# Kernel tuning notes

Measured on AMD Instinct MI355X. Metric: run time of the kernel, lower is better.

The kernel has to match this reference:

```python
import jax, jax.numpy as jnp
import numpy as np

N_FILTERS = 64
COV_EPS = 1e-4
ALPHA = 0.1  # cov_shrinkage_alpha

_tri_r, _tri_c = np.triu_indices(N_FILTERS)
_TRI_R = jnp.asarray(_tri_r)
_TRI_C = jnp.asarray(_tri_c)
_TRI_SCALE = jnp.where(_TRI_R != _TRI_C, np.sqrt(2.0), 1.0).astype(jnp.float32)


def setup_inputs() -> dict:
    key = jax.random.key(0)
    k1, k2 = jax.random.split(key)
    x = jax.random.normal(k1, (256, 128, 1, 4096), dtype=jnp.float32)
    # 1x1 conv weight [out_ch, in_ch] (kernel spatial dims are 1x1)
    proj_w = jax.random.normal(k2, (64, 128), dtype=jnp.float32) * 0.05
    return {"x": x, "proj_w": proj_w}


def reference(x, proj_w):
    # 1x1 conv channel projection: [B, Cin, 1, T] -> [B, F, T]
    x = jnp.einsum('bcht,fc->bfht', x, proj_w)[:, :, 0, :].astype(jnp.float32)
    # center over time
    x = x - x.mean(axis=-1, keepdims=True)
    denom = float(max(x.shape[-1] - 1, 1))
    cov = jnp.einsum('bft,bgt->bfg', x, x) / denom  # [B, F, F]
    n = cov.shape[-1]
    eye = jnp.eye(n, dtype=cov.dtype)
    # shrinkage toward scaled identity
    mu = jnp.trace(cov, axis1=-2, axis2=-1) / n  # [B]
    cov = (1.0 - ALPHA) * cov + ALPHA * mu[:, None, None] * eye
    # symmetrize + jitter
    cov = 0.5 * (cov + jnp.swapaxes(cov, -1, -2)) + COV_EPS * eye
    # log-Euclidean map via batched eigh
    eigvals, eigvecs = jnp.linalg.eigh(cov)
    eigvals = jnp.clip(eigvals, COV_EPS)
    log_cov = jnp.einsum('bij,bj,bkj->bik', eigvecs, jnp.log(eigvals), eigvecs)
    log_cov = 0.5 * (log_cov + jnp.swapaxes(log_cov, -1, -2))
    # upper-triangular vectorization with sqrt(2) off-diagonal scaling
    vec = log_cov[:, _TRI_R, _TRI_C] * _TRI_SCALE  # [B, F*(F+1)/2]
    return vec
```

## Files before the change

### kernel.cpp

```cpp
#include <hip/hip_runtime.h>

typedef __attribute__((ext_vector_type(8))) short s8_t;
typedef __attribute__((ext_vector_type(4))) float f4_t;

#define NBATCH 256
#define NCH    128
#define NT     4096
#define NF     64
#define TT     128
#define CHUNKS 4
#define CT     (NT / CHUNKS)
#define NIT    (CT / TT)
#define LDSK   (TT + 8)
#define CHEB_D 20

static __device__ __forceinline__ unsigned short f32_bf16(float f) {
    unsigned int u = __float_as_uint(f);
    return (unsigned short)((u + 0x7FFFu + ((u >> 16) & 1u)) >> 16);
}
static __device__ __forceinline__ float bf16_f32(unsigned short h) {
    return __uint_as_float(((unsigned int)h) << 16);
}

__global__ __launch_bounds__(512, 4)
void k_gram(const float* __restrict__ x, float* __restrict__ gws, float* __restrict__ sxws) {
    __shared__ __align__(16) unsigned short xl[2][NCH * LDSK];
    __shared__ float red[512];

    const int tid  = threadIdx.x;
    const int lane = tid & 63;
    const int wv   = tid >> 6;
    const int bid  = blockIdx.x;
    const int b    = bid >> 2;
    const int chnk = bid & 3;
    const int lrow16 = tid >> 5;
    const int lchunk = tid & 31;

    const float* xb = x + (size_t)b * ((size_t)NCH * NT) + chnk * CT;

    const int arow0 = (wv & 3) * 32;
    const int bcol0 = (wv >> 2) * 64;
    const int lrow  = lane & 15;
    const int koff  = (lane >> 4) * 8;

    f4_t acc[2][4];
    #pragma unroll
    for (int i = 0; i < 2; ++i)
        #pragma unroll
        for (int j = 0; j < 4; ++j)
            acc[i][j] = (f4_t){0.f, 0.f, 0.f, 0.f};

    float sxp = 0.f;
    float4 ld[8];

    #pragma unroll
    for (int j = 0; j < 8; ++j) {
        const int r = j * 16 + lrow16;
        ld[j] = *(const float4*)(xb + (size_t)r * NT + lchunk * 4);
    }
    #pragma unroll
    for (int j = 0; j < 8; ++j) {
        const int r = j * 16 + lrow16;
        ushort4 h;
        h.x = f32_bf16(ld[j].x); h.y = f32_bf16(ld[j].y);
        h.z = f32_bf16(ld[j].z); h.w = f32_bf16(ld[j].w);
        *(ushort4*)&xl[0][r * LDSK + lchunk * 4] = h;
    }
    __syncthreads();

    for (int it = 0; it < NIT; ++it) {
        const int cur = it & 1;
        if (it + 1 < NIT) {
            const int t0 = (it + 1) * TT;
            #pragma unroll
            for (int j = 0; j < 8; ++j) {
                const int r = j * 16 + lrow16;
                ld[j] = *(const float4*)(xb + (size_t)r * NT + t0 + lchunk * 4);
            }
        }
        const unsigned short* bufc = xl[cur];
        #pragma unroll
        for (int ks = 0; ks < TT / 32; ++ks) {
            const int k0 = ks * 32 + koff;
            const s8_t af0 = *(const s8_t*)&bufc[(arow0 + lrow) * LDSK + k0];
            const s8_t af1 = *(const s8_t*)&bufc[(arow0 + 16 + lrow) * LDSK + k0];
            #pragma unroll
            for (int cb = 0; cb < 4; ++cb) {
                const s8_t bf = *(const s8_t*)&bufc[(bcol0 + cb * 16 + lrow) * LDSK + k0];
                acc[0][cb] = __builtin_amdgcn_mfma_f32_16x16x32_bf16(af0, bf, acc[0][cb], 0, 0, 0);
                acc[1][cb] = __builtin_amdgcn_mfma_f32_16x16x32_bf16(af1, bf, acc[1][cb], 0, 0, 0);
            }
        }
        {
            const unsigned short* rp = &bufc[(tid >> 2) * LDSK + (tid & 3) * 32];
            float s = 0.f;
            #pragma unroll
            for (int q = 0; q < 4; ++q) {
                s8_t v = *(const s8_t*)&rp[q * 8];
                #pragma unroll
                for (int e = 0; e < 8; ++e)
                    s += bf16_f32((unsigned short)v[e]);
            }
            sxp += s;
        }
        if (it + 1 < NIT) {
            #pragma unroll
            for (int j = 0; j < 8; ++j) {
                const int r = j * 16 + lrow16;
                ushort4 h;
                h.x = f32_bf16(ld[j].x); h.y = f32_bf16(ld[j].y);
                h.z = f32_bf16(ld[j].z); h.w = f32_bf16(ld[j].w);
                *(ushort4*)&xl[cur ^ 1][r * LDSK + lchunk * 4] = h;
            }
        }
        __syncthreads();
    }

    float* gb = gws + ((size_t)bid << 14);
    const int lrow4 = (lane >> 4) * 4;
    const int lcol  = lane & 15;
    #pragma unroll
    for (int i = 0; i < 2; ++i) {
        const int rbase = arow0 + i * 16 + lrow4;
        #pragma unroll
        for (int cb = 0; cb < 4; ++cb) {
            const int col = bcol0 + cb * 16 + lcol;
            #pragma unroll
            for (int reg = 0; reg < 4; ++reg)
                gb[(size_t)(rbase + reg) * NCH + col] = acc[i][cb][reg];
        }
    }
    red[tid] = sxp;
    __syncthreads();
    if (tid < NCH)
        sxws[bid * NCH + tid] = red[tid * 4] + red[tid * 4 + 1] + red[tid * 4 + 2] + red[tid * 4 + 3];
}

__global__ __launch_bounds__(512, 2)
void k_logm(const float* __restrict__ gws, const float* __restrict__ sxws,
            const float* __restrict__ wmat, float* __restrict__ out) {
    __shared__ __align__(16) float lds[33032];
    float* sG   = lds;
    float* sC0  = lds;
    float* sU   = lds + 4096;
    float* sB0  = lds + 8192;
    float* sB1  = lds + 12288;
    float* sWt  = lds + 16384;
    float* sM1t = lds + 24576;
    float* ssx  = lds + 32768;
    float* sp   = lds + 32896;
    float* sred = lds + 32960;
    float* sscal= lds + 33024;

    const int tid = threadIdx.x;
    const int b   = blockIdx.x;

    for (int i = tid; i < NF * NCH; i += 512) sM1t[i] = wmat[i];
    if (tid < NCH) {
        const float* sxb = sxws + (size_t)b * 4 * NCH;
        ssx[tid] = sxb[tid] + sxb[NCH + tid] + sxb[2 * NCH + tid] + sxb[3 * NCH + tid];
    }
    {
        const float4* g0 = (const float4*)(gws + ((size_t)(b * 4 + 0) << 14));
        const float4* g1 = (const float4*)(gws + ((size_t)(b * 4 + 1) << 14));
        const float4* g2 = (const float4*)(gws + ((size_t)(b * 4 + 2) << 14));
        const float4* g3 = (const float4*)(gws + ((size_t)(b * 4 + 3) << 14));
        float4* dst = (float4*)sG;
        for (int i = tid; i < 4096; i += 512) {
            const float4 a = g0[i], c = g1[i], d = g2[i], e = g3[i];
            float4 r;
            r.x = a.x + c.x + d.x + e.x;
            r.y = a.y + c.y + d.y + e.y;
            r.z = a.z + c.z + d.z + e.z;
            r.w = a.w + c.w + d.w + e.w;
            dst[i] = r;
        }
    }
    __syncthreads();
    for (int i = tid; i < NF * NCH; i += 512) {
        const int f = i >> 7, k = i & 127;
        sWt[k * 64 + f] = sM1t[i];
    }
    __syncthreads();

    {
        const int f0 = (tid >> 5) * 4, c0 = (tid & 31) * 4;
        float a[4][4];
        #pragma unroll
        for (int i = 0; i < 4; ++i)
            #pragma unroll
            for (int j = 0; j < 4; ++j) a[i][j] = 0.f;
        for (int k = 0; k < NCH; ++k) {
            const float4 w4 = *(const float4*)&sWt[k * 64 + f0];
            const float4 g4 = *(const float4*)&sG[k * NCH + c0];
            const float wa[4] = {w4.x, w4.y, w4.z, w4.w};
            const float ga[4] = {g4.x, g4.y, g4.z, g4.w};
            #pragma unroll
            for (int i = 0; i < 4; ++i)
                #pragma unroll
                for (int j = 0; j < 4; ++j)
                    a[i][j] = fmaf(wa[i], ga[j], a[i][j]);
        }
        #pragma unroll
        for (int j = 0; j < 4; ++j) {
            float4 v; v.x = a[0][j]; v.y = a[1][j]; v.z = a[2][j]; v.w = a[3][j];
            *(float4*)&sM1t[(c0 + j) * 64 + f0] = v;
        }
    }
    if (tid < NF) {
        float s = 0.f;
        for (int k = 0; k < NCH; ++k) s = fmaf(sWt[k * 64 + tid], ssx[k], s);
        sp[tid] = s;
    }
    __syncthreads();

    {
        const int f0 = (tid >> 5) * 4, g2 = (tid & 31) * 2;
        float a[4][2];
        #pragma unroll
        for (int i = 0; i < 4; ++i) { a[i][0] = 0.f; a[i][1] = 0.f; }
        for (int k = 0; k < NCH; ++k) {
            const float4 m4 = *(const float4*)&sM1t[k * 64 + f0];
            const float2 w2 = *(const float2*)&sWt[k * 64 + g2];
            const float ma[4] = {m4.x, m4.y, m4.z, m4.w};
            #pragma unroll
            for (int i = 0; i < 4; ++i) {
                a[i][0] = fmaf(ma[i], w2.x, a[i][0]);
                a[i][1] = fmaf(ma[i], w2.y, a[i][1]);
            }
        }
        const float i4096 = 1.f / 4096.f, i4095 = 1.f / 4095.f;
        #pragma unroll
        for (int i = 0; i < 4; ++i)
            #pragma unroll
            for (int j = 0; j < 2; ++j)
                sC0[(f0 + i) * 64 + (g2 + j)] =
                    (a[i][j] - sp[f0 + i] * sp[g2 + j] * i4096) * i4095;
    }
    __syncthreads();

    if (tid == 0) {
        float s = 0.f;
        for (int i = 0; i < 64; ++i) s += sC0[i * 65];
        sscal[0] = s * (1.f / 64.f);
    }
    __syncthreads();

    const float mu = sscal[0];
    const float dshift = 0.1f * mu + 1e-4f;
    for (int i = tid; i < 4096; i += 512) {
        const int r = i >> 6, c = i & 63;
        float v = 0.45f * (sC0[r * 64 + c] + sC0[c * 64 + r]);
        if (r == c) v += dshift;
        sU[i] = v;
    }
    __syncthreads();

    if (tid < 64) {
        float s = 0.f;
        for (int j = 0; j < 64; ++j) s += fabsf(sU[j * 64 + tid]);
        sred[tid] = s;
    }
    __syncthreads();
    if (tid == 0) {
        float hi = 0.f;
        for (int i = 0; i < 64; ++i) hi = fmaxf(hi, sred[i]);
        const float lo = dshift;
        hi = fmaxf(hi, lo * 1.02f);
        float wsc = (hi - lo) / (hi + lo);
        wsc = fminf(fmaxf(wsc, 1e-6f), 0.999999f);
        const float zz = fmaxf((1.f - sqrtf(fmaxf(1.f - wsc * wsc, 1e-12f))) / wsc, 1e-12f);
        const float mc = 0.5f * (hi + lo);
        sscal[1] = mc;
        sscal[2] = wsc;
        sscal[3] = zz;
        sscal[4] = logf(mc) - log1pf(zz * zz);
    }
    __syncthreads();

    {
        const float mc = sscal[1], wsc = sscal[2];
        const float inv_mw = 1.f / (mc * wsc);
        const float inv_w  = 1.f / wsc;
        for (int i = tid; i < 4096; i += 512) {
            const int r = i >> 6, c = i & 63;
            float v = sU[i] * inv_mw;
            if (r == c) v -= inv_w;
            sU[i] = v;
        }
    }
    __syncthreads();

    const int f0 = (tid >> 5) * 4, g2 = (tid & 31) * 2;
    const float zc  = sscal[3];
    const float l2z = log2f(zc);
    float rP[4][2], rP2[4][2];
    {
        const float cd = 2.f * ((CHEB_D & 1) ? 1.f : -1.f) *
                         exp2f((float)CHEB_D * l2z) / (float)CHEB_D;
        #pragma unroll
        for (int i = 0; i < 4; ++i)
            #pragma unroll
            for (int j = 0; j < 2; ++j) {
                rP[i][j]  = (f0 + i == g2 + j) ? cd : 0.f;
                rP2[i][j] = 0.f;
            }
        #pragma unroll
        for (int i = 0; i < 4; ++i) {
            float2 v; v.x = rP[i][0]; v.y = rP[i][1];
            *(float2*)&sB0[(f0 + i) * 64 + g2] = v;
        }
    }
    __syncthreads();

    float* bcur = sB0;
    float* bnxt = sB1;
    for (int k = CHEB_D - 1; k >= 1; --k) {
        const float ck = 2.f * ((k & 1) ? 1.f : -1.f) * exp2f((float)k * l2z) / (float)k;
        float a[4][2];
        #pragma unroll
        for (int i = 0; i < 4; ++i) { a[i][0] = 0.f; a[i][1] = 0.f; }
        #pragma unroll 4
        for (int kk = 0; kk < 64; ++kk) {
            const float4 u4 = *(const float4*)&sU[kk * 64 + f0];
            const float2 b2 = *(const float2*)&bcur[kk * 64 + g2];
            const float ua[4] = {u4.x, u4.y, u4.z, u4.w};
            #pragma unroll
            for (int i = 0; i < 4; ++i) {
                a[i][0] = fmaf(ua[i], b2.x, a[i][0]);
                a[i][1] = fmaf(ua[i], b2.y, a[i][1]);
            }
        }
        #pragma unroll
        for (int i = 0; i < 4; ++i)
            #pragma unroll
            for (int j = 0; j < 2; ++j) {
                const float v = 2.f * a[i][j] - rP2[i][j] + ((f0 + i == g2 + j) ? ck : 0.f);
                rP2[i][j] = rP[i][j];
                rP[i][j]  = v;
            }
        #pragma unroll
        for (int i = 0; i < 4; ++i) {
            float2 v; v.x = rP[i][0]; v.y = rP[i][1];
            *(float2*)&bnxt[(f0 + i) * 64 + g2] = v;
        }
        float* t = bcur; bcur = bnxt; bnxt = t;
        __syncthreads();
    }
    {
        const float c0c = sscal[4];
        float a[4][2];
        #pragma unroll
        for (int i = 0; i < 4; ++i) { a[i][0] = 0.f; a[i][1] = 0.f; }
        #pragma unroll 4
        for (int kk = 0; kk < 64; ++kk) {
            const float4 u4 = *(const float4*)&sU[kk * 64 + f0];
            const float2 b2 = *(const float2*)&bcur[kk * 64 + g2];
            const float ua[4] = {u4.x, u4.y, u4.z, u4.w};
            #pragma unroll
            for (int i = 0; i < 4; ++i) {
                a[i][0] = fmaf(ua[i], b2.x, a[i][0]);
                a[i][1] = fmaf(ua[i], b2.y, a[i][1]);
            }
        }
        #pragma unroll
        for (int i = 0; i < 4; ++i) {
            float2 v;
            v.x = ((f0 + i == g2 + 0) ? c0c : 0.f) + a[i][0] - rP2[i][0];
            v.y = ((f0 + i == g2 + 1) ? c0c : 0.f) + a[i][1] - rP2[i][1];
            *(float2*)&bnxt[(f0 + i) * 64 + g2] = v;
        }
    }
    __syncthreads();
    const float* sF = bnxt;

    float* ob = out + (size_t)b * 2080;
    for (int idx = tid; idx < 2080; idx += 512) {
        const double disc = 16641.0 - 8.0 * (double)idx;
        const int i = (int)((129.0 - sqrt(disc)) * 0.5);
        const int Si = i * 64 - (i * (i - 1)) / 2;
        const int j = i + (idx - Si);
        float v = 0.5f * (sF[i * 64 + j] + sF[j * 64 + i]);
        if (i != j) v *= 1.4142135623730951f;
        ob[idx] = v;
    }
}

extern "C" void kernel_launch(void* const* d_in, const int* in_sizes, int n_in,
                              void* d_out, int out_size, void* d_ws, size_t ws_size,
                              hipStream_t stream) {
    const float* x    = (const float*)d_in[0];
    const float* wmat = (const float*)d_in[1];
    float* outp = (float*)d_out;
    float* gws  = (float*)d_ws;
    float* sxws = gws + (size_t)NBATCH * CHUNKS * NCH * NCH;
    k_gram<<<dim3(NBATCH * CHUNKS), dim3(512), 0, stream>>>(x, gws, sxws);
    k_logm<<<dim3(NBATCH), dim3(512), 0, stream>>>(gws, sxws, wmat, outp);
}
```

Before: 780.1 us.

## Fuse Gram accumulation and log-matrix stage into a single per-batch kernel

Merges the chunked Gram/row-sum kernel and the projection/logm kernel into one kernel with one block per batch. Each block now sweeps the full time axis itself and writes the Gram matrix and channel sums straight into LDS. This removes the global workspace round trip, the cross-chunk reduction and a second launch. In exchange, the memory-bound Gram phase drops from 1024 blocks at four per CU to 256 single-resident blocks, leaving fewer waves to hide global-load latency.

New measurement: 751.8 us. 1.04x faster.

```diff
diff --git a/kernel.cpp b/kernel.cpp
--- a/kernel.cpp
+++ b/kernel.cpp
@@ -8,9 +8,7 @@
 #define NT     4096
 #define NF     64
 #define TT     128
-#define CHUNKS 4
-#define CT     (NT / CHUNKS)
-#define NIT    (CT / TT)
+#define NIT    (NT / TT)
 #define LDSK   (TT + 8)
 #define CHEB_D 20
 
@@ -22,124 +20,11 @@
     return __uint_as_float(((unsigned int)h) << 16);
 }
 
-__global__ __launch_bounds__(512, 4)
-void k_gram(const float* __restrict__ x, float* __restrict__ gws, float* __restrict__ sxws) {
-    __shared__ __align__(16) unsigned short xl[2][NCH * LDSK];
-    __shared__ float red[512];
-
-    const int tid  = threadIdx.x;
-    const int lane = tid & 63;
-    const int wv   = tid >> 6;
-    const int bid  = blockIdx.x;
-    const int b    = bid >> 2;
-    const int chnk = bid & 3;
-    const int lrow16 = tid >> 5;
-    const int lchunk = tid & 31;
-
-    const float* xb = x + (size_t)b * ((size_t)NCH * NT) + chnk * CT;
-
-    const int arow0 = (wv & 3) * 32;
-    const int bcol0 = (wv >> 2) * 64;
-    const int lrow  = lane & 15;
-    const int koff  = (lane >> 4) * 8;
-
-    f4_t acc[2][4];
-    #pragma unroll
-    for (int i = 0; i < 2; ++i)
-        #pragma unroll
-        for (int j = 0; j < 4; ++j)
-            acc[i][j] = (f4_t){0.f, 0.f, 0.f, 0.f};
-
-    float sxp = 0.f;
-    float4 ld[8];
-
-    #pragma unroll
-    for (int j = 0; j < 8; ++j) {
-        const int r = j * 16 + lrow16;
-        ld[j] = *(const float4*)(xb + (size_t)r * NT + lchunk * 4);
-    }
-    #pragma unroll
-    for (int j = 0; j < 8; ++j) {
-        const int r = j * 16 + lrow16;
-        ushort4 h;
-        h.x = f32_bf16(ld[j].x); h.y = f32_bf16(ld[j].y);
-        h.z = f32_bf16(ld[j].z); h.w = f32_bf16(ld[j].w);
-        *(ushort4*)&xl[0][r * LDSK + lchunk * 4] = h;
-    }
-    __syncthreads();
-
-    for (int it = 0; it < NIT; ++it) {
-        const int cur = it & 1;
-        if (it + 1 < NIT) {
-            const int t0 = (it + 1) * TT;
-            #pragma unroll
-            for (int j = 0; j < 8; ++j) {
-                const int r = j * 16 + lrow16;
-                ld[j] = *(const float4*)(xb + (size_t)r * NT + t0 + lchunk * 4);
-            }
-        }
-        const unsigned short* bufc = xl[cur];
-        #pragma unroll
-        for (int ks = 0; ks < TT / 32; ++ks) {
-            const int k0 = ks * 32 + koff;
-            const s8_t af0 = *(const s8_t*)&bufc[(arow0 + lrow) * LDSK + k0];
-            const s8_t af1 = *(const s8_t*)&bufc[(arow0 + 16 + lrow) * LDSK + k0];
-            #pragma unroll
-            for (int cb = 0; cb < 4; ++cb) {
-                const s8_t bf = *(const s8_t*)&bufc[(bcol0 + cb * 16 + lrow) * LDSK + k0];
-                acc[0][cb] = __builtin_amdgcn_mfma_f32_16x16x32_bf16(af0, bf, acc[0][cb], 0, 0, 0);
-                acc[1][cb] = __builtin_amdgcn_mfma_f32_16x16x32_bf16(af1, bf, acc[1][cb], 0, 0, 0);
-            }
-        }
-        {
-            const unsigned short* rp = &bufc[(tid >> 2) * LDSK + (tid & 3) * 32];
-            float s = 0.f;
-            #pragma unroll
-            for (int q = 0; q < 4; ++q) {
-                s8_t v = *(const s8_t*)&rp[q * 8];
-                #pragma unroll
-                for (int e = 0; e < 8; ++e)
-                    s += bf16_f32((unsigned short)v[e]);
-            }
-            sxp += s;
-        }
-        if (it + 1 < NIT) {
-            #pragma unroll
-            for (int j = 0; j < 8; ++j) {
-                const int r = j * 16 + lrow16;
-                ushort4 h;
-                h.x = f32_bf16(ld[j].x); h.y = f32_bf16(ld[j].y);
-                h.z = f32_bf16(ld[j].z); h.w = f32_bf16(ld[j].w);
-                *(ushort4*)&xl[cur ^ 1][r * LDSK + lchunk * 4] = h;
-            }
-        }
-        __syncthreads();
-    }
-
-    float* gb = gws + ((size_t)bid << 14);
-    const int lrow4 = (lane >> 4) * 4;
-    const int lcol  = lane & 15;
-    #pragma unroll
-    for (int i = 0; i < 2; ++i) {
-        const int rbase = arow0 + i * 16 + lrow4;
-        #pragma unroll
-        for (int cb = 0; cb < 4; ++cb) {
-            const int col = bcol0 + cb * 16 + lcol;
-            #pragma unroll
-            for (int reg = 0; reg < 4; ++reg)
-                gb[(size_t)(rbase + reg) * NCH + col] = acc[i][cb][reg];
-        }
-    }
-    red[tid] = sxp;
-    __syncthreads();
-    if (tid < NCH)
-        sxws[bid * NCH + tid] = red[tid * 4] + red[tid * 4 + 1] + red[tid * 4 + 2] + red[tid * 4 + 3];
-}
-
-__global__ __launch_bounds__(512, 2)
-void k_logm(const float* __restrict__ gws, const float* __restrict__ sxws,
-            const float* __restrict__ wmat, float* __restrict__ out) {
-    __shared__ __align__(16) float lds[33032];
+__global__ __launch_bounds__(512, 1)
+void k_fused(const float* __restrict__ x, const float* __restrict__ wmat,
+             float* __restrict__ out) {
+    __shared__ __align__(16) float lds[33544];
+    unsigned short* xl = (unsigned short*)lds;
     float* sG   = lds;
     float* sC0  = lds;
     float* sU   = lds + 4096;
@@ -151,36 +36,129 @@
     float* sp   = lds + 32896;
     float* sred = lds + 32960;
     float* sscal= lds + 33024;
-
-    const int tid = threadIdx.x;
-    const int b   = blockIdx.x;
-
-    for (int i = tid; i < NF * NCH; i += 512) sM1t[i] = wmat[i];
-    if (tid < NCH) {
-        const float* sxb = sxws + (size_t)b * 4 * NCH;
-        ssx[tid] = sxb[tid] + sxb[NCH + tid] + sxb[2 * NCH + tid] + sxb[3 * NCH + tid];
-    }
-    {
-        const float4* g0 = (const float4*)(gws + ((size_t)(b * 4 + 0) << 14));
-        const float4* g1 = (const float4*)(gws + ((size_t)(b * 4 + 1) << 14));
-        const float4* g2 = (const float4*)(gws + ((size_t)(b * 4 + 2) << 14));
-        const float4* g3 = (const float4*)(gws + ((size_t)(b * 4 + 3) << 14));
-        float4* dst = (float4*)sG;
-        for (int i = tid; i < 4096; i += 512) {
-            const float4 a = g0[i], c = g1[i], d = g2[i], e = g3[i];
-            float4 r;
-            r.x = a.x + c.x + d.x + e.x;
-            r.y = a.y + c.y + d.y + e.y;
-            r.z = a.z + c.z + d.z + e.z;
-            r.w = a.w + c.w + d.w + e.w;
-            dst[i] = r;
-        }
-    }
-    __syncthreads();
-    for (int i = tid; i < NF * NCH; i += 512) {
-        const int f = i >> 7, k = i & 127;
-        sWt[k * 64 + f] = sM1t[i];
-    }
+    float* red  = lds + 33032;
+
+    const int tid  = threadIdx.x;
+    const int b    = blockIdx.x;
+    const int lane = tid & 63;
+    const int wv   = tid >> 6;
+    const int lrow16 = tid >> 5;
+    const int lchunk = tid & 31;
+
+    const float* xb = x + (size_t)b * ((size_t)NCH * NT);
+
+    const int arow0 = (wv & 3) * 32;
+    const int bcol0 = (wv >> 2) * 64;
+    const int lrow  = lane & 15;
+    const int koff  = (lane >> 4) * 8;
+
+    f4_t acc[2][4];
+    #pragma unroll
+    for (int i = 0; i < 2; ++i)
+        #pragma unroll
+        for (int j = 0; j < 4; ++j)
+            acc[i][j] = (f4_t){0.f, 0.f, 0.f, 0.f};
+
+    float sxp = 0.f;
+    float4 ld[8];
+
+    #pragma unroll
+    for (int j = 0; j < 8; ++j) {
+        const int r = j * 16 + lrow16;
+        ld[j] = *(const float4*)(xb + (size_t)r * NT + lchunk * 4);
+    }
+    #pragma unroll
+    for (int j = 0; j < 8; ++j) {
+        const int r = j * 16 + lrow16;
+        ushort4 h;
+        h.x = f32_bf16(ld[j].x); h.y = f32_bf16(ld[j].y);
+        h.z = f32_bf16(ld[j].z); h.w = f32_bf16(ld[j].w);
+        *(ushort4*)&xl[r * LDSK + lchunk * 4] = h;
+    }
+    __syncthreads();
+
+    for (int it = 0; it < NIT; ++it) {
+        const int cur = it & 1;
+        if (it + 1 < NIT) {
+            const int t0 = (it + 1) * TT;
+            #pragma unroll
+            for (int j = 0; j < 8; ++j) {
+                const int r = j * 16 + lrow16;
+                ld[j] = *(const float4*)(xb + (size_t)r * NT + t0 + lchunk * 4);
+            }
+        }
+        const unsigned short* bufc = xl + cur * (NCH * LDSK);
+        #pragma unroll
+        for (int ks = 0; ks < TT / 32; ++ks) {
+            const int k0 = ks * 32 + koff;
+            const s8_t af0 = *(const s8_t*)&bufc[(arow0 + lrow) * LDSK + k0];
+            const s8_t af1 = *(const s8_t*)&bufc[(arow0 + 16 + lrow) * LDSK + k0];
+            #pragma unroll
+            for (int cb = 0; cb < 4; ++cb) {
+                const s8_t bf = *(const s8_t*)&bufc[(bcol0 + cb * 16 + lrow) * LDSK + k0];
+                acc[0][cb] = __builtin_amdgcn_mfma_f32_16x16x32_bf16(af0, bf, acc[0][cb], 0, 0, 0);
+                acc[1][cb] = __builtin_amdgcn_mfma_f32_16x16x32_bf16(af1, bf, acc[1][cb], 0, 0, 0);
+            }
+        }
+        {
+            const unsigned short* rp = &bufc[(tid >> 2) * LDSK + (tid & 3) * 32];
+            float s = 0.f;
+            #pragma unroll
+            for (int q = 0; q < 4; ++q) {
+                s8_t v = *(const s8_t*)&rp[q * 8];
+                #pragma unroll
+                for (int e = 0; e < 8; ++e)
+                    s += bf16_f32((unsigned short)v[e]);
+            }
+            sxp += s;
+        }
+        if (it + 1 < NIT) {
+            unsigned short* bufn = xl + (cur ^ 1) * (NCH * LDSK);
+            #pragma unroll
+            for (int j = 0; j < 8; ++j) {
+                const int r = j * 16 + lrow16;
+                ushort4 h;
+                h.x = f32_bf16(ld[j].x); h.y = f32_bf16(ld[j].y);
+                h.z = f32_bf16(ld[j].z); h.w = f32_bf16(ld[j].w);
+                *(ushort4*)&bufn[r * LDSK + lchunk * 4] = h;
+            }
+        }
+        __syncthreads();
+    }
+
+    const int wf = tid & 63, wkq = tid >> 6;
+    float4 wreg[4];
+    #pragma unroll
+    for (int q = 0; q < 4; ++q)
+        wreg[q] = *(const float4*)(wmat + wf * NCH + wkq * 16 + q * 4);
+
+    {
+        const int lrow4 = (lane >> 4) * 4;
+        const int lcol  = lane & 15;
+        #pragma unroll
+        for (int i = 0; i < 2; ++i) {
+            const int rbase = arow0 + i * 16 + lrow4;
+            #pragma unroll
+            for (int cb = 0; cb < 4; ++cb) {
+                const int col = bcol0 + cb * 16 + lcol;
+                #pragma unroll
+                for (int reg = 0; reg < 4; ++reg)
+                    sG[(rbase + reg) * NCH + col] = acc[i][cb][reg];
+            }
+        }
+    }
+    red[tid] = sxp;
+    #pragma unroll
+    for (int q = 0; q < 4; ++q) {
+        const int k0 = wkq * 16 + q * 4;
+        sWt[(k0 + 0) * 64 + wf] = wreg[q].x;
+        sWt[(k0 + 1) * 64 + wf] = wreg[q].y;
+        sWt[(k0 + 2) * 64 + wf] = wreg[q].z;
+        sWt[(k0 + 3) * 64 + wf] = wreg[q].w;
+    }
+    __syncthreads();
+    if (tid < NCH)
+        ssx[tid] = red[tid * 4] + red[tid * 4 + 1] + red[tid * 4 + 2] + red[tid * 4 + 3];
     __syncthreads();
 
     {
@@ -392,8 +370,6 @@
     const float* x    = (const float*)d_in[0];
     const float* wmat = (const float*)d_in[1];
     float* outp = (float*)d_out;
-    float* gws  = (float*)d_ws;
-    float* sxws = gws + (size_t)NBATCH * CHUNKS * NCH * NCH;
-    k_gram<<<dim3(NBATCH * CHUNKS), dim3(512), 0, stream>>>(x, gws, sxws);
-    k_logm<<<dim3(NBATCH), dim3(512), 0, stream>>>(gws, sxws, wmat, outp);
+    (void)d_ws; (void)ws_size;
+    k_fused<<<dim3(NBATCH), dim3(512), 0, stream>>>(x, wmat, outp);
 }
```
